# Optimization experiments

Measured on AMD Instinct MI355X. Metric: run time of the kernel, lower is better.

Reference implementation:

```python
import jax, jax.numpy as jnp
import numpy as np

N_NODES = 100000
N_EDGES = 1250000
IN_DIM = 128
HID = 64


def gcn_conv(x, W, b, src, dst, n_nodes):
    # PyG GCNConv: h = D^{-1/2} (A + I) D^{-1/2} (X W) + b
    h = x @ W  # [N, out]
    loop = jnp.arange(n_nodes)
    s = jnp.concatenate([src, loop])
    d = jnp.concatenate([dst, loop])
    deg = jnp.zeros((n_nodes,), h.dtype).at[d].add(1.0)
    dinv = jnp.where(deg > 0, deg ** -0.5, 0.0)
    norm = dinv[s] * dinv[d]  # [E+N]
    msgs = h[s] * norm[:, None]  # irregular gather, memory-bound
    out = jax.ops.segment_sum(msgs, d, num_segments=n_nodes)
    return out + b


def setup_inputs() -> dict:
    key = jax.random.key(0)
    ks = jax.random.split(key, 4)
    x = jax.random.normal(ks[0], (N_NODES, IN_DIM), jnp.float32)
    edge_index = jax.random.randint(ks[1], (2, N_EDGES), 0, N_NODES, jnp.int64)
    # Glorot-ish init for linear weights
    W1 = jax.random.normal(ks[2], (IN_DIM, HID), jnp.float32) * (1.0 / np.sqrt(IN_DIM))
    b1 = jnp.zeros((HID,), jnp.float32)
    W2 = jax.random.normal(ks[3], (HID, HID), jnp.float32) * (1.0 / np.sqrt(HID))
    b2 = jnp.zeros((HID,), jnp.float32)
    return {"x": x, "edge_index": edge_index, "W1": W1, "b1": b1, "W2": W2, "b2": b2}


def reference(x, edge_index, W1, b1, W2, b2):
    n_nodes = x.shape[0]
    src, dst = edge_index[0], edge_index[1]
    h = gcn_conv(x, W1, b1, src, dst, n_nodes)
    h = jax.nn.relu(h)  # dropout is identity in eval mode
    h = gcn_conv(h, W2, b2, src, dst, n_nodes)
    return h
```

## Files before the change

### kernel.cpp

```cpp
#include <hip/hip_runtime.h>
#include <hip/hip_fp16.h>

constexpr int NN = 100000;
constexpr int NE = 1250000;
constexpr int KDIM = 128;
constexpr int HID = 64;

constexpr int NPB = 128;
constexpr int NB  = (NN + NPB - 1) / NPB;
constexpr int NBP = 1024;
constexpr int CAP = 2048;
constexpr int BIN_BLOCKS = 256;
constexpr int BIN_CHUNK  = (NE + BIN_BLOCKS - 1) / BIN_BLOCKS;
constexpr int EPT = (BIN_CHUNK + 1023) / 1024;

using half8   = __attribute__((ext_vector_type(8))) _Float16;
using floatx4 = __attribute__((ext_vector_type(4))) float;

__global__ __launch_bounds__(256) void k_prep(const float* __restrict__ W1,
                                              const float* __restrict__ W2,
                                              __half* __restrict__ Whp1,
                                              __half* __restrict__ Whp2,
                                              int* __restrict__ gcur) {
    const int blk = blockIdx.x;
    if (blk < 4) {
        int t = blk * 256 + threadIdx.x;
        int lane = t & 63, frag = t >> 6;
        int ks = frag >> 2, ct = frag & 3;
        int quad = lane >> 4, n = lane & 15;
        __half tmp[8];
#pragma unroll
        for (int j = 0; j < 8; ++j)
            tmp[j] = __float2half(W1[(ks * 32 + quad * 8 + j) * HID + ct * 16 + n]);
        *(uint4*)(Whp1 + t * 8) = *(uint4*)tmp;
    } else if (blk < 6) {
        int t = (blk - 4) * 256 + threadIdx.x;
        int lane = t & 63, frag = t >> 6;
        int ks = frag >> 2, ct = frag & 3;
        int quad = lane >> 4, n = lane & 15;
        __half tmp[8];
#pragma unroll
        for (int j = 0; j < 8; ++j)
            tmp[j] = __float2half(W2[(ks * 32 + quad * 8 + j) * HID + ct * 16 + n]);
        *(uint4*)(Whp2 + t * 8) = *(uint4*)tmp;
    } else {
        for (int i = threadIdx.x; i < NBP; i += 256) gcur[i] = 0;
    }
}

__global__ __launch_bounds__(1024) void k_bin(const int* __restrict__ src,
                                              const int* __restrict__ dst,
                                              int* __restrict__ gcur,
                                              unsigned* __restrict__ pack1) {
    __shared__ int cnt[NBP], rnk[NBP], gbase[NBP];
    const int t = threadIdx.x;
    for (int i = t; i < NBP; i += 1024) { cnt[i] = 0; rnk[i] = 0; }
    __syncthreads();
    const int c0 = blockIdx.x * BIN_CHUNK;
    int b[EPT];
    unsigned val[EPT];
#pragma unroll
    for (int i = 0; i < EPT; ++i) {
        int idx = i * 1024 + t;
        int e = c0 + idx;
        b[i] = -1;
        if (idx < BIN_CHUNK && e < NE) {
            int d = dst[e], s = src[e];
            int bb = d >> 7;
            b[i] = bb;
            val[i] = (unsigned)s | ((unsigned)(d & 127) << 17);
            atomicAdd(&cnt[bb], 1);
        }
    }
    __syncthreads();
    for (int i = t; i < NBP; i += 1024) {
        int c = cnt[i];
        if (c) gbase[i] = i * CAP + atomicAdd(&gcur[i], c);
    }
    __syncthreads();
#pragma unroll
    for (int i = 0; i < EPT; ++i) {
        if (b[i] >= 0) {
            int r = atomicAdd(&rnk[b[i]], 1);
            pack1[gbase[b[i]] + r] = val[i];
        }
    }
}

__global__ __launch_bounds__(256) void k_sort(const unsigned* __restrict__ pack1,
                                              const int* __restrict__ gcur,
                                              unsigned* __restrict__ pack2,
                                              int* __restrict__ row_start,
                                              int* __restrict__ deg,
                                              float* __restrict__ dinv) {
    __shared__ int h[NPB];
    __shared__ int sh[NPB];
    const int t = threadIdx.x;
    const int bkt = blockIdx.x;
    if (t < NPB) h[t] = 0;
    __syncthreads();
    const int beg = bkt * CAP, end = beg + gcur[bkt];
    for (int i = beg + t; i < end; i += 256)
        atomicAdd(&h[(pack1[i] >> 17) & 127], 1);
    __syncthreads();
    int v0 = 0;
    if (t < NPB) { v0 = h[t]; sh[t] = v0; }
    __syncthreads();
    int val = v0;
    for (int off = 1; off < NPB; off <<= 1) {
        int add = (t < NPB && t >= off) ? sh[t - off] : 0;
        __syncthreads();
        if (t < NPB) { val += add; sh[t] = val; }
        __syncthreads();
    }
    if (t < NPB) {
        int start = beg + (val - v0);
        int node = bkt * NPB + t;
        if (node < NN) {
            row_start[node] = start;
            deg[node] = v0;
            dinv[node] = rsqrtf((float)(v0 + 1));
        }
        h[t] = start;
    }
    __syncthreads();
    for (int i = beg + t; i < end; i += 256) {
        unsigned p = pack1[i];
        int pos = atomicAdd(&h[(p >> 17) & 127], 1);
        pack2[pos] = p & 0x1FFFF;
    }
}

template <int K>
__global__ __launch_bounds__(256) void k_mm(const float* __restrict__ x,
                                            const __half* __restrict__ Whp,
                                            const float* __restrict__ dinv,
                                            __half* __restrict__ gout) {
    const int t = threadIdx.x;
    const int w = t >> 6, lane = t & 63;
    const int quad = lane >> 4, m = lane & 15;
    const int rowA = blockIdx.x * 64 + w * 16 + m;
    const bool rok = rowA < NN;
    const float* xr = x + (long)rowA * K + quad * 8;

    floatx4 acc[4] = {};
#pragma unroll
    for (int ks = 0; ks < K / 32; ++ks) {
        float xv[8];
        if (rok) {
            float4 p0 = *(const float4*)(xr + ks * 32);
            float4 p1 = *(const float4*)(xr + ks * 32 + 4);
            xv[0] = p0.x; xv[1] = p0.y; xv[2] = p0.z; xv[3] = p0.w;
            xv[4] = p1.x; xv[5] = p1.y; xv[6] = p1.z; xv[7] = p1.w;
        } else {
#pragma unroll
            for (int j = 0; j < 8; ++j) xv[j] = 0.f;
        }
        half8 a;
#pragma unroll
        for (int j = 0; j < 8; ++j) a[j] = (_Float16)xv[j];
#pragma unroll
        for (int ct = 0; ct < 4; ++ct) {
            half8 b = *(const half8*)(Whp + ((ks * 4 + ct) * 64 + lane) * 8);
            acc[ct] = __builtin_amdgcn_mfma_f32_16x16x32_f16(a, b, acc[ct], 0, 0, 0);
        }
    }

#pragma unroll
    for (int r = 0; r < 4; ++r) {
        int rowD = blockIdx.x * 64 + w * 16 + quad * 4 + r;
        if (rowD < NN) {
            float dv = dinv[rowD];
#pragma unroll
            for (int ct = 0; ct < 4; ++ct)
                gout[rowD * HID + ct * 16 + m] = __float2half(dv * acc[ct][r]);
        }
    }
}

__global__ __launch_bounds__(256) void k_aggmm(const unsigned* __restrict__ pack2,
                                               const int* __restrict__ row_start,
                                               const int* __restrict__ deg,
                                               const float* __restrict__ dinv,
                                               const __half* __restrict__ g1,
                                               const float* __restrict__ b1,
                                               const __half* __restrict__ Whp2,
                                               __half* __restrict__ g2) {
    __shared__ __half tile[16][72];
    const int w = threadIdx.x >> 6, lane = threadIdx.x & 63;
    const int sub = lane & 15, slot = lane >> 4;
    const int vbase = blockIdx.x * 16 + w * 4;
    const float4 bv = *(const float4*)(b1 + sub * 4);

    int4   rs4 = *(const int4*)(row_start + vbase);
    int4   dg4 = *(const int4*)(deg + vbase);
    float4 dv4 = *(const float4*)(dinv + vbase);
    const int   beg_i[4] = {rs4.x, rs4.y, rs4.z, rs4.w};
    const int   cnt_i[4] = {dg4.x, dg4.y, dg4.z, dg4.w};
    const float dv_i[4]  = {dv4.x, dv4.y, dv4.z, dv4.w};
    int pre[4];
#pragma unroll
    for (int i = 0; i < 4; ++i) {
        pre[i] = 0;
        if (lane < cnt_i[i]) pre[i] = (int)pack2[beg_i[i] + lane];
    }

#pragma unroll
    for (int i = 0; i < 4; ++i) {
        const int v = vbase + i;
        const int beg = beg_i[i];
        const int cnt = cnt_i[i];
        const int n0 = cnt < 64 ? cnt : 64;
        float4 acc = make_float4(0.f, 0.f, 0.f, 0.f);

        int k = 0;
        for (; k + 8 <= n0; k += 8) {
            int sA = __shfl(pre[i], k + slot);
            int sB = __shfl(pre[i], k + 4 + slot);
            uint2 rA = *(const uint2*)(g1 + sA * HID + sub * 4);
            uint2 rB = *(const uint2*)(g1 + sB * HID + sub * 4);
            float2 a0 = __half22float2(*(const __half2*)&rA.x);
            float2 a1 = __half22float2(*(const __half2*)&rA.y);
            float2 b0 = __half22float2(*(const __half2*)&rB.x);
            float2 b1f = __half22float2(*(const __half2*)&rB.y);
            acc.x += a0.x + b0.x; acc.y += a0.y + b0.y;
            acc.z += a1.x + b1f.x; acc.w += a1.y + b1f.y;
        }
        for (; k < n0; k += 4) {
            int idx  = k + slot;
            int idxc = idx < n0 ? idx : 0;
            int s = __shfl(pre[i], idxc);
            if (idx < n0) {
                uint2 r = *(const uint2*)(g1 + s * HID + sub * 4);
                float2 a0 = __half22float2(*(const __half2*)&r.x);
                float2 a1 = __half22float2(*(const __half2*)&r.y);
                acc.x += a0.x; acc.y += a0.y; acc.z += a1.x; acc.w += a1.y;
            }
        }
        for (int kk = 64 + slot; kk < cnt; kk += 4) {
            int s = (int)pack2[beg + kk];
            uint2 r = *(const uint2*)(g1 + s * HID + sub * 4);
            float2 a0 = __half22float2(*(const __half2*)&r.x);
            float2 a1 = __half22float2(*(const __half2*)&r.y);
            acc.x += a0.x; acc.y += a0.y; acc.z += a1.x; acc.w += a1.y;
        }
#pragma unroll
        for (int mm = 16; mm <= 32; mm <<= 1) {
            acc.x += __shfl_xor(acc.x, mm);
            acc.y += __shfl_xor(acc.y, mm);
            acc.z += __shfl_xor(acc.z, mm);
            acc.w += __shfl_xor(acc.w, mm);
        }
        if (slot == 0) {
            const float dv = dv_i[i];
            uint2 sr = *(const uint2*)(g1 + v * HID + sub * 4);
            float2 s0 = __half22float2(*(const __half2*)&sr.x);
            float2 s1 = __half22float2(*(const __half2*)&sr.y);
            __half tmp[4];
            tmp[0] = __float2half(fmaxf(dv * (acc.x + s0.x) + bv.x, 0.f));
            tmp[1] = __float2half(fmaxf(dv * (acc.y + s0.y) + bv.y, 0.f));
            tmp[2] = __float2half(fmaxf(dv * (acc.z + s1.x) + bv.z, 0.f));
            tmp[3] = __float2half(fmaxf(dv * (acc.w + s1.y) + bv.w, 0.f));
            *(uint2*)&tile[w * 4 + i][sub * 4] = *(uint2*)tmp;
        }
    }
    __syncthreads();

    const int quad = lane >> 4, m = lane & 15;
    floatx4 acc2 = {};
#pragma unroll
    for (int ks = 0; ks < 2; ++ks) {
        half8 a = *(const half8*)&tile[m][ks * 32 + quad * 8];
        half8 b = *(const half8*)(Whp2 + ((ks * 4 + w) * 64 + lane) * 8);
        acc2 = __builtin_amdgcn_mfma_f32_16x16x32_f16(a, b, acc2, 0, 0, 0);
    }
#pragma unroll
    for (int r = 0; r < 4; ++r) {
        int rowD = blockIdx.x * 16 + quad * 4 + r;
        g2[rowD * HID + w * 16 + m] = __float2half(dinv[rowD] * acc2[r]);
    }
}

__global__ __launch_bounds__(256) void k_agg(const unsigned* __restrict__ pack2,
                                             const int* __restrict__ row_start,
                                             const int* __restrict__ deg,
                                             const float* __restrict__ dinv,
                                             const __half* __restrict__ g,
                                             const float* __restrict__ bias,
                                             float* __restrict__ out) {
    const int v = blockIdx.x * 4 + (threadIdx.x >> 6);
    if (v >= NN) return;
    const int lane = threadIdx.x & 63;
    const int sub  = lane & 15;
    const int slot = lane >> 4;
    const int beg = row_start[v];
    const int cnt = deg[v];
    int pre = 0;
    if (lane < cnt) pre = (int)pack2[beg + lane];
    const int n0 = cnt < 64 ? cnt : 64;
    float4 acc = make_float4(0.f, 0.f, 0.f, 0.f);

    int k = 0;
    for (; k + 8 <= n0; k += 8) {
        int sA = __shfl(pre, k + slot);
        int sB = __shfl(pre, k + 4 + slot);
        uint2 rA = *(const uint2*)(g + sA * HID + sub * 4);
        uint2 rB = *(const uint2*)(g + sB * HID + sub * 4);
        float2 a0 = __half22float2(*(const __half2*)&rA.x);
        float2 a1 = __half22float2(*(const __half2*)&rA.y);
        float2 b0 = __half22float2(*(const __half2*)&rB.x);
        float2 b1 = __half22float2(*(const __half2*)&rB.y);
        acc.x += a0.x + b0.x; acc.y += a0.y + b0.y;
        acc.z += a1.x + b1.x; acc.w += a1.y + b1.y;
    }
    for (; k < n0; k += 4) {
        int idx  = k + slot;
        int idxc = idx < n0 ? idx : 0;
        int s = __shfl(pre, idxc);
        if (idx < n0) {
            uint2 r = *(const uint2*)(g + s * HID + sub * 4);
            float2 a0 = __half22float2(*(const __half2*)&r.x);
            float2 a1 = __half22float2(*(const __half2*)&r.y);
            acc.x += a0.x; acc.y += a0.y; acc.z += a1.x; acc.w += a1.y;
        }
    }
    for (int kk = 64 + slot; kk < cnt; kk += 4) {
        int s = (int)pack2[beg + kk];
        uint2 r = *(const uint2*)(g + s * HID + sub * 4);
        float2 a0 = __half22float2(*(const __half2*)&r.x);
        float2 a1 = __half22float2(*(const __half2*)&r.y);
        acc.x += a0.x; acc.y += a0.y; acc.z += a1.x; acc.w += a1.y;
    }
#pragma unroll
    for (int mm = 16; mm <= 32; mm <<= 1) {
        acc.x += __shfl_xor(acc.x, mm);
        acc.y += __shfl_xor(acc.y, mm);
        acc.z += __shfl_xor(acc.z, mm);
        acc.w += __shfl_xor(acc.w, mm);
    }
    if (slot == 0) {
        const float dv = dinv[v];
        uint2 sr = *(const uint2*)(g + v * HID + sub * 4);
        float2 s0 = __half22float2(*(const __half2*)&sr.x);
        float2 s1 = __half22float2(*(const __half2*)&sr.y);
        float4 bv = *(const float4*)(bias + sub * 4);
        float4 o;
        o.x = dv * (acc.x + s0.x) + bv.x;
        o.y = dv * (acc.y + s0.y) + bv.y;
        o.z = dv * (acc.z + s1.x) + bv.z;
        o.w = dv * (acc.w + s1.y) + bv.w;
        *(float4*)(out + v * HID + sub * 4) = o;
    }
}

extern "C" void kernel_launch(void* const* d_in, const int* in_sizes, int n_in,
                              void* d_out, int out_size, void* d_ws, size_t ws_size,
                              hipStream_t stream) {
    const float* x  = (const float*)d_in[0];
    const int*   ei = (const int*)d_in[1];
    const float* W1 = (const float*)d_in[2];
    const float* b1 = (const float*)d_in[3];
    const float* W2 = (const float*)d_in[4];
    const float* b2 = (const float*)d_in[5];
    float* out = (float*)d_out;
    (void)in_sizes; (void)n_in; (void)out_size; (void)ws_size;

    const int* src = ei;
    const int* dst = ei + NE;

    char* ws = (char*)d_ws;
    int*      gcur      = (int*)(ws + 0x000000);
    __half*   Whp1      = (__half*)(ws + 0x004000);
    __half*   Whp2      = (__half*)(ws + 0x008000);
    float*    dinv      = (float*)(ws + 0x010000);
    int*      row_start = (int*)(ws + 0x080000);
    int*      deg       = (int*)(ws + 0x100000);
    unsigned* pack1     = (unsigned*)(ws + 0x200000);
    unsigned* pack2     = (unsigned*)(ws + 0xA00000);
    __half*   g1        = (__half*)(ws + 0x1200000);
    __half*   g2        = (__half*)(ws + 0x2000000);

    k_prep<<<7, 256, 0, stream>>>(W1, W2, Whp1, Whp2, gcur);
    k_bin<<<BIN_BLOCKS, 1024, 0, stream>>>(src, dst, gcur, pack1);
    k_sort<<<NB, 256, 0, stream>>>(pack1, gcur, pack2, row_start, deg, dinv);

    k_mm<KDIM><<<(NN + 63) / 64, 256, 0, stream>>>(x, Whp1, dinv, g1);
    k_aggmm<<<NN / 16, 256, 0, stream>>>(pack2, row_start, deg, dinv, g1, b1, Whp2, g2);
    k_agg<<<(NN + 3) / 4, 256, 0, stream>>>(pack2, row_start, deg, dinv, g2, b2, out);
}
```

Measured before the change: 209.4 us.

## Replace two-pass bucketed CSR build with count, scan, atomic scatter

Replaces the block-binned edge packing and per-bucket local sort with a classic CSR build: global atomic degree count, a single-block prefix scan over all nodes, and a global atomic scatter of source indices. This removes the intermediate pack1 buffer and the bucket capacity limit. In exchange it uses heavy global atomics on random destinations and a serial single-block scan, and edge order within each row becomes nondeterministic.

```diff
diff --git a/kernel.cpp b/kernel.cpp
--- a/kernel.cpp
+++ b/kernel.cpp
@@ -6,14 +6,6 @@
 constexpr int KDIM = 128;
 constexpr int HID = 64;
 
-constexpr int NPB = 128;
-constexpr int NB  = (NN + NPB - 1) / NPB;
-constexpr int NBP = 1024;
-constexpr int CAP = 2048;
-constexpr int BIN_BLOCKS = 256;
-constexpr int BIN_CHUNK  = (NE + BIN_BLOCKS - 1) / BIN_BLOCKS;
-constexpr int EPT = (BIN_CHUNK + 1023) / 1024;
-
 using half8   = __attribute__((ext_vector_type(8))) _Float16;
 using floatx4 = __attribute__((ext_vector_type(4))) float;
 
@@ -21,7 +13,7 @@
                                               const float* __restrict__ W2,
                                               __half* __restrict__ Whp1,
                                               __half* __restrict__ Whp2,
-                                              int* __restrict__ gcur) {
+                                              int* __restrict__ deg) {
     const int blk = blockIdx.x;
     if (blk < 4) {
         int t = blk * 256 + threadIdx.x;
@@ -44,90 +36,56 @@
             tmp[j] = __float2half(W2[(ks * 32 + quad * 8 + j) * HID + ct * 16 + n]);
         *(uint4*)(Whp2 + t * 8) = *(uint4*)tmp;
     } else {
-        for (int i = threadIdx.x; i < NBP; i += 256) gcur[i] = 0;
-    }
-}
-
-__global__ __launch_bounds__(1024) void k_bin(const int* __restrict__ src,
-                                              const int* __restrict__ dst,
-                                              int* __restrict__ gcur,
-                                              unsigned* __restrict__ pack1) {
-    __shared__ int cnt[NBP], rnk[NBP], gbase[NBP];
+        for (int i = (blk - 6) * 256 + threadIdx.x; i < NN; i += 64 * 256)
+            deg[i] = 0;
+    }
+}
+
+__global__ __launch_bounds__(256) void k_count(const int* __restrict__ dst,
+                                               int* __restrict__ deg) {
+    const int e = blockIdx.x * 256 + threadIdx.x;
+    if (e < NE) atomicAdd(&deg[dst[e]], 1);
+}
+
+__global__ __launch_bounds__(1024) void k_scan(const int* __restrict__ deg,
+                                               int* __restrict__ row_start,
+                                               int* __restrict__ cur,
+                                               float* __restrict__ dinv) {
+    __shared__ int sh[1024];
     const int t = threadIdx.x;
-    for (int i = t; i < NBP; i += 1024) { cnt[i] = 0; rnk[i] = 0; }
+    const int lo = t * 98;
+    const int hi = (lo + 98 < NN) ? lo + 98 : NN;
+    int s = 0;
+    for (int v = lo; v < hi; ++v) s += deg[v];
+    sh[t] = s;
     __syncthreads();
-    const int c0 = blockIdx.x * BIN_CHUNK;
-    int b[EPT];
-    unsigned val[EPT];
-#pragma unroll
-    for (int i = 0; i < EPT; ++i) {
-        int idx = i * 1024 + t;
-        int e = c0 + idx;
-        b[i] = -1;
-        if (idx < BIN_CHUNK && e < NE) {
-            int d = dst[e], s = src[e];
-            int bb = d >> 7;
-            b[i] = bb;
-            val[i] = (unsigned)s | ((unsigned)(d & 127) << 17);
-            atomicAdd(&cnt[bb], 1);
-        }
-    }
-    __syncthreads();
-    for (int i = t; i < NBP; i += 1024) {
-        int c = cnt[i];
-        if (c) gbase[i] = i * CAP + atomicAdd(&gcur[i], c);
-    }
-    __syncthreads();
-#pragma unroll
-    for (int i = 0; i < EPT; ++i) {
-        if (b[i] >= 0) {
-            int r = atomicAdd(&rnk[b[i]], 1);
-            pack1[gbase[b[i]] + r] = val[i];
-        }
-    }
-}
-
-__global__ __launch_bounds__(256) void k_sort(const unsigned* __restrict__ pack1,
-                                              const int* __restrict__ gcur,
-                                              unsigned* __restrict__ pack2,
-                                              int* __restrict__ row_start,
-                                              int* __restrict__ deg,
-                                              float* __restrict__ dinv) {
-    __shared__ int h[NPB];
-    __shared__ int sh[NPB];
-    const int t = threadIdx.x;
-    const int bkt = blockIdx.x;
-    if (t < NPB) h[t] = 0;
-    __syncthreads();
-    const int beg = bkt * CAP, end = beg + gcur[bkt];
-    for (int i = beg + t; i < end; i += 256)
-        atomicAdd(&h[(pack1[i] >> 17) & 127], 1);
-    __syncthreads();
-    int v0 = 0;
-    if (t < NPB) { v0 = h[t]; sh[t] = v0; }
-    __syncthreads();
-    int val = v0;
-    for (int off = 1; off < NPB; off <<= 1) {
-        int add = (t < NPB && t >= off) ? sh[t - off] : 0;
+    int val = s;
+    for (int off = 1; off < 1024; off <<= 1) {
+        int add = (t >= off) ? sh[t - off] : 0;
         __syncthreads();
-        if (t < NPB) { val += add; sh[t] = val; }
+        val += add;
+        sh[t] = val;
         __syncthreads();
     }
-    if (t < NPB) {
-        int start = beg + (val - v0);
-        int node = bkt * NPB + t;
-        if (node < NN) {
-            row_start[node] = start;
-            deg[node] = v0;
-            dinv[node] = rsqrtf((float)(v0 + 1));
-        }
-        h[t] = start;
-    }
-    __syncthreads();
-    for (int i = beg + t; i < end; i += 256) {
-        unsigned p = pack1[i];
-        int pos = atomicAdd(&h[(p >> 17) & 127], 1);
-        pack2[pos] = p & 0x1FFFF;
+    int run = val - s;
+    for (int v = lo; v < hi; ++v) {
+        int d = deg[v];
+        row_start[v] = run;
+        cur[v] = run;
+        dinv[v] = rsqrtf((float)(d + 1));
+        run += d;
+    }
+    if (t == 0) row_start[NN] = NE;
+}
+
+__global__ __launch_bounds__(256) void k_scatter(const int* __restrict__ src,
+                                                 const int* __restrict__ dst,
+                                                 int* __restrict__ cur,
+                                                 unsigned* __restrict__ pack2) {
+    const int e = blockIdx.x * 256 + threadIdx.x;
+    if (e < NE) {
+        int pos = atomicAdd(&cur[dst[e]], 1);
+        pack2[pos] = (unsigned)src[e];
     }
 }
 
@@ -369,20 +327,20 @@
     const int* dst = ei + NE;
 
     char* ws = (char*)d_ws;
-    int*      gcur      = (int*)(ws + 0x000000);
     __half*   Whp1      = (__half*)(ws + 0x004000);
     __half*   Whp2      = (__half*)(ws + 0x008000);
     float*    dinv      = (float*)(ws + 0x010000);
     int*      row_start = (int*)(ws + 0x080000);
     int*      deg       = (int*)(ws + 0x100000);
-    unsigned* pack1     = (unsigned*)(ws + 0x200000);
-    unsigned* pack2     = (unsigned*)(ws + 0xA00000);
+    int*      cur       = (int*)(ws + 0x180000);
+    unsigned* pack2     = (unsigned*)(ws + 0x200000);
     __half*   g1        = (__half*)(ws + 0x1200000);
     __half*   g2        = (__half*)(ws + 0x2000000);
 
-    k_prep<<<7, 256, 0, stream>>>(W1, W2, Whp1, Whp2, gcur);
-    k_bin<<<BIN_BLOCKS, 1024, 0, stream>>>(src, dst, gcur, pack1);
-    k_sort<<<NB, 256, 0, stream>>>(pack1, gcur, pack2, row_start, deg, dinv);
+    k_prep<<<70, 256, 0, stream>>>(W1, W2, Whp1, Whp2, deg);
+    k_count<<<(NE + 255) / 256, 256, 0, stream>>>(dst, deg);
+    k_scan<<<1, 1024, 0, stream>>>(deg, row_start, cur, dinv);
+    k_scatter<<<(NE + 255) / 256, 256, 0, stream>>>(src, dst, cur, pack2);
 
     k_mm<KDIM><<<(NN + 63) / 64, 256, 0, stream>>>(x, Whp1, dinv, g1);
     k_aggmm<<<NN / 16, 256, 0, stream>>>(pack2, row_start, deg, dinv, g1, b1, Whp2, g2);
```

After: 596.6 us. +184.9%, slower.
